# Performance work log

Measured on AMD Instinct MI355X. Metric: run time of the kernel, lower is better.

Reference implementation:

```python
import jax, jax.numpy as jnp
import numpy as np


def setup_inputs() -> dict:
    B, L, D, M, S = 4, 1024, 1024, 16, 8
    key = jax.random.key(0)
    ks = jax.random.split(key, 12)
    sd = 0.02
    inp = {
        "hid": jax.random.normal(ks[0], (B, L, D), jnp.float32),
        "src_hid": jax.random.normal(ks[1], (B, L, D), jnp.float32),
        "sp_width": jax.random.randint(ks[2], (B, L), 0, 9),
        "max_sp_len": S,
        "attention_mask": jnp.ones((B, L), bool),
        "src_mask": jnp.ones((B, L), bool),
        # span-start attention (1 head): query/key linears + relative-key embedding table
        "wq_st": sd * jax.random.normal(ks[3], (D, D), jnp.float32),
        "bq_st": jnp.zeros((D,), jnp.float32),
        "wk_st": sd * jax.random.normal(ks[4], (D, D), jnp.float32),
        "bk_st": jnp.zeros((D,), jnp.float32),
        "rel_st": sd * jax.random.normal(ks[5], (2 * M + 1, D), jnp.float32),
        # span-end attention
        "wq_ed": sd * jax.random.normal(ks[6], (D, D), jnp.float32),
        "bq_ed": jnp.zeros((D,), jnp.float32),
        "wk_ed": sd * jax.random.normal(ks[7], (D, D), jnp.float32),
        "bk_ed": jnp.zeros((D,), jnp.float32),
        "rel_ed": sd * jax.random.normal(ks[8], (2 * M + 1, D), jnp.float32),
        # sp_emb: Linear(2D -> D), stored as [2D, D] (x @ W + b)
        "sp_w": sd * jax.random.normal(ks[9], (2 * D, D), jnp.float32),
        "sp_b": jnp.zeros((D,), jnp.float32),
    }
    return inp


def reference(hid, src_hid, sp_width, max_sp_len, attention_mask, src_mask,
              wq_st, bq_st, wk_st, bk_st, rel_st,
              wq_ed, bq_ed, wk_ed, bk_ed, rel_ed, sp_w, sp_b):
    B, L, D = hid.shape
    scale = 1.0 / jnp.sqrt(jnp.float32(D))
    M = (rel_st.shape[0] - 1) // 2
    pos = jnp.arange(L)
    rel_idx = jnp.clip(pos[None, :] - pos[:, None], -M, M) + M          # [L,L]
    rel_idx_b = jnp.broadcast_to(rel_idx[None], (B, L, L))

    amask = (src_mask[:, :, None] & attention_mask[:, None, :]).astype(jnp.float32)  # [B,Lq,Lk]
    attn_w0 = amask / jnp.clip(jnp.sum(amask, 2, keepdims=True), 1e-6)

    def attn(query, wq, bq, wk, bk, rel_tab, mask):
        # single-head relative-position attention; returns attention weights [B,L,L]
        q = (query @ wq + bq) * scale                                   # [B,L,D]
        k = hid @ wk + bk                                               # [B,L,D]
        sc = jnp.einsum('bqd,bkd->bqk', q, k)
        # q . rel_emb[rel_idx[q_pos,k_pos]]: contract with table then gather (avoids [L,L,D])
        rel_sc = jnp.take_along_axis(jnp.einsum('bqd,rd->bqr', q, rel_tab), rel_idx_b, axis=2)
        sc = jnp.where(mask > 0, sc + rel_sc, -1e18)
        return jax.nn.softmax(sc, axis=-1)

    def upd(attn_w, hidp):
        # weighted sum of hid + linear + relu (dropout is identity in eval)
        hidc = jnp.einsum('bqk,bkd->bqd', attn_w, hid)
        return jax.nn.relu(jnp.concatenate([hidp, hidc], axis=2) @ sp_w + sp_b)

    sts, eds, masks = [attn_w0], [attn_w0], []
    hid1, hid2 = src_hid, src_hid
    for i in range(max_sp_len):
        m = (i < sp_width).astype(jnp.float32)                          # [B,L]
        masks.append(m)
        mask_i = m[:, :, None] * amask                                  # [B,L,L]
        hid1 = upd(sts[-1], hid1)
        sts.append(attn(hid1, wq_st, bq_st, wk_st, bk_st, rel_st, mask_i))
        hid2 = upd(eds[-1], hid2)
        eds.append(attn(hid2, wq_ed, bq_ed, wk_ed, bk_ed, rel_ed, mask_i))

    return (jnp.stack(sts[1:], -2),   # [B,L,S,L]
            jnp.stack(eds[1:], -2),   # [B,L,S,L]
            jnp.stack(masks, -1))     # [B,L,S]
```

## Files before the change

kernel.cpp:

```cpp
#include <hip/hip_runtime.h>

typedef unsigned short u16;
typedef __attribute__((ext_vector_type(8))) short bh8;
typedef __attribute__((ext_vector_type(4))) float f4;

__device__ __forceinline__ u16 f2b(float x){
  union { float f; unsigned u; } c; c.f = x;
  unsigned r = (c.u + 0x7FFFu + ((c.u >> 16) & 1u)) >> 16;
  return (u16)r;
}
__device__ __forceinline__ float b2f(u16 h){
  union { unsigned u; float f; } c; c.u = ((unsigned)h) << 16; return c.f;
}
__device__ __forceinline__ void gload16(const void* g, void* l){
  __builtin_amdgcn_global_load_lds((const __attribute__((address_space(1))) void*)g,
                                   (__attribute__((address_space(3))) void*)l, 16, 0, 0);
}


__global__ __launch_bounds__(256) void convall_k(const float* __restrict__ hid,
                                                 const float* __restrict__ wq0, const float* __restrict__ wq1,
                                                 const float* __restrict__ wk0, const float* __restrict__ wk1,
                                                 u16* __restrict__ hidB, u16* __restrict__ wqB, u16* __restrict__ wkB){
  long i = (long)blockIdx.x*256 + threadIdx.x;
  const float* src; u16* dst; long off;
  if      (i < 4194304L){ src = hid; dst = hidB;           off = i; }
  else if (i < 5242880L){ src = wq0; dst = wqB;            off = i - 4194304L; }
  else if (i < 6291456L){ src = wq1; dst = wqB + 1048576;  off = i - 5242880L; }
  else if (i < 7340032L){ src = wk0; dst = wkB;            off = i - 6291456L; }
  else                  { src = wk1; dst = wkB + 1048576;  off = i - 7340032L; }
  dst[off] = f2b(src[off]);
}

__global__ __launch_bounds__(256) void uniform0_k(const int* __restrict__ spw, float* __restrict__ out){
  int bl = blockIdx.x;
  if (spw[bl] != 0) return;
  f4 t = {0.0009765625f, 0.0009765625f, 0.0009765625f, 0.0009765625f};
  float* b0 = out + (size_t)bl*8192;
  float* b1 = out + 33554432ull + (size_t)bl*8192;
  #pragma unroll
  for (int i = 0; i < 8; i++){
    ((f4*)(b0 + (size_t)i*1024))[threadIdx.x] = t;
    ((f4*)(b1 + (size_t)i*1024))[threadIdx.x] = t;
  }
}

__global__ __launch_bounds__(256) void trans_k(const float* __restrict__ in, u16* __restrict__ out,
                                               int R, int C){
  __shared__ u16 t[32][33];
  int bx = blockIdx.x*32, by = blockIdx.y*32;
  int tx = threadIdx.x & 31, ty = threadIdx.x >> 5;
  #pragma unroll
  for (int j = 0; j < 32; j += 8) t[ty+j][tx] = f2b(in[(size_t)(by+ty+j)*C + bx+tx]);
  __syncthreads();
  #pragma unroll
  for (int j = 0; j < 32; j += 8) out[(size_t)(bx+ty+j)*R + by+tx] = t[tx][ty+j];
}

__global__ __launch_bounds__(256) void sort_k(const int* __restrict__ spw, int* __restrict__ perm,
                                              int* __restrict__ cnt, float* __restrict__ mout){
  int b = blockIdx.x, t = threadIdx.x;
  __shared__ int hist[9], start[9];
  if (t < 9) hist[t] = 0;
  __syncthreads();
  for (int l = t; l < 1024; l += 256) atomicAdd(&hist[spw[b*1024 + l]], 1);
  __syncthreads();
  if (t == 0){
    int acc = 0;
    for (int w = 8; w >= 0; w--){ start[w] = acc; acc += hist[w]; }
  }
  __syncthreads();
  if (t < 8) cnt[b*8 + t] = start[t];
  __syncthreads();
  for (int l = t; l < 1024; l += 256){
    int w = spw[b*1024 + l];
    float* mo = mout + ((size_t)b*1024 + l)*8;
    #pragma unroll
    for (int i = 0; i < 8; i++) mo[i] = (i < w) ? 1.0f : 0.0f;
    int pos = atomicAdd(&start[w], 1);
    perm[b*1024 + pos] = l;
  }
}

__global__ __launch_bounds__(256) void gather_k(const float* __restrict__ srch, const int* __restrict__ perm,
                                                u16* __restrict__ hb){
  int blk = blockIdx.x;
  int z = blk >> 10, c = blk & 1023;
  int ro = perm[z*1024 + c];
  const float* src = srch + ((size_t)z*1024 + ro)*1024;
  u16* dst = hb + ((size_t)z*1024 + c)*1024;
  for (int d = threadIdx.x; d < 1024; d += 256) dst[d] = f2b(src[d]);
}

__global__ __launch_bounds__(256) void wrt_k(const float* __restrict__ wq0, const float* __restrict__ wq1,
                                             const float* __restrict__ rel0, const float* __restrict__ rel1,
                                             u16* __restrict__ Mx){
  long idx = (long)blockIdx.x*256 + threadIdx.x;
  if (idx >= 2L*33*1024) return;
  int s = idx >= 33*1024; long loc = idx - (s ? 33*1024 : 0);
  int r = (int)(loc >> 10), e = (int)(loc & 1023);
  const float* wqrow = (s ? wq1 : wq0) + (size_t)e*1024;
  const float* rel = (s ? rel1 : rel0) + (size_t)r*1024;
  float acc = 0.0f;
  #pragma unroll 4
  for (int k = 0; k < 1024; k++) acc += wqrow[k]*rel[k];
  u16 v = f2b(acc*0.03125f);
  size_t o = (size_t)(1024 + r)*1024 + e;
  #pragma unroll
  for (int b = 0; b < 4; b++)
    Mx[(size_t)(s*4 + b)*1179648 + o] = v;
}

__global__ __launch_bounds__(256) void dots_k(const float* __restrict__ wq0, const float* __restrict__ wq1,
                                              const float* __restrict__ wk0, const float* __restrict__ wk1,
                                              const float* __restrict__ bq0, const float* __restrict__ bq1,
                                              const float* __restrict__ bk0, const float* __restrict__ bk1,
                                              const float* __restrict__ rel0, const float* __restrict__ rel1,
                                              float* __restrict__ ubuf, float* __restrict__ c0buf,
                                              float* __restrict__ bqbk, float* __restrict__ cba){
  int row = blockIdx.x*4 + (threadIdx.x >> 6);
  int lane = threadIdx.x & 63;
  if (row >= 4164) return;
  const float *a, *v;
  int kind = 0, oi = 0, br_s = 0, br_r = 0;
  if      (row < 1024){ a = wk0 + (size_t)row*1024; v = bq0; oi = row; }
  else if (row < 2048){ a = wk1 + (size_t)(row-1024)*1024; v = bq1; oi = row; }
  else if (row < 3072){ a = wq0 + (size_t)(row-2048)*1024; v = bk0; kind = 1; oi = row-2048; }
  else if (row < 4096){ a = wq1 + (size_t)(row-3072)*1024; v = bk1; kind = 1; oi = row-3072+1024; }
  else if (row < 4162){ int idx = row-4096; br_s = idx/33; br_r = idx%33;
                        a = (br_s ? rel1 : rel0) + (size_t)br_r*1024; v = br_s ? bq1 : bq0; kind = 2; }
  else                { int s2 = row-4162; a = s2 ? bq1 : bq0; v = s2 ? bk1 : bk0; kind = 3; oi = s2; }
  const f4* ap = (const f4*)a;
  const f4* vp = (const f4*)v;
  float acc = 0.0f;
  #pragma unroll
  for (int p = 0; p < 4; p++){
    f4 x = ap[lane + 64*p], y = vp[lane + 64*p];
    acc += x[0]*y[0] + x[1]*y[1] + x[2]*y[2] + x[3]*y[3];
  }
  #pragma unroll
  for (int off = 32; off > 0; off >>= 1) acc += __shfl_xor(acc, off, 64);
  if (lane == 0){
    if (kind == 0) ubuf[oi] = acc;
    else if (kind == 1) c0buf[oi] = acc;
    else if (kind == 2){
      float w = acc*0.03125f;
      for (int b = 0; b < 4; b++) cba[(br_s*4 + b)*1152 + 1024 + br_r] = w;
    } else bqbk[oi] = acc;
  }
}

__global__ __launch_bounds__(256) void cba_k(const float* __restrict__ hid, const float* __restrict__ u,
                                             const float* __restrict__ bqbk, float* __restrict__ cba){
  int row = blockIdx.x*4 + (threadIdx.x >> 6);
  int lane = threadIdx.x & 63;
  int z = row >> 10, l = row & 1023, b = z & 3, s = z >> 2;
  const f4* hp = (const f4*)(hid + ((size_t)b*1024 + l)*1024);
  const f4* up = (const f4*)(u + s*1024);
  float acc = 0.0f;
  #pragma unroll
  for (int p = 0; p < 4; p++){
    f4 a = hp[lane + 64*p], c = up[lane + 64*p];
    acc += a[0]*c[0] + a[1]*c[1] + a[2]*c[2] + a[3]*c[3];
  }
  #pragma unroll
  for (int off = 32; off > 0; off >>= 1) acc += __shfl_xor(acc, off, 64);
  if (!lane) cba[z*1152 + l] = (acc + bqbk[s])*0.03125f;
}

__global__ __launch_bounds__(256) void meanh2_k(const u16* __restrict__ H2T, float* __restrict__ mh){
  int row = blockIdx.x*4 + (threadIdx.x >> 6);
  int lane = threadIdx.x & 63;
  const u16* p = H2T + (size_t)row*1024 + lane*16;
  float s = 0.0f;
  #pragma unroll
  for (int j = 0; j < 16; j++) s += b2f(p[j]);
  #pragma unroll
  for (int off = 32; off > 0; off >>= 1) s += __shfl_xor(s, off, 64);
  if (lane == 0) mh[row] = s * 0.0009765625f;
}

__global__ __launch_bounds__(256) void softmax_k(const u16* __restrict__ scB, float* __restrict__ outF,
                                                 u16* __restrict__ attnP, const float* __restrict__ qrelb,
                                                 const int* __restrict__ cnt, const int* __restrict__ perm,
                                                 const int* __restrict__ spw, int iter){
  int z = blockIdx.x >> 10, c = blockIdx.x & 1023;
  int s = z >> 2, b = z & 3;
  if (c >= cnt[b*8 + iter]) return;
  int ro = perm[b*1024 + c];
  __shared__ float qr[33];
  __shared__ float red[8];
  if (threadIdx.x < 33) qr[threadIdx.x] = qrelb[((size_t)z*1024 + c)*33 + threadIdx.x];
  __syncthreads();
  const u16* sc = scB + ((size_t)z*1024 + c)*1024;
  float* po = outF + (size_t)s*33554432ull + (((size_t)(b*1024 + ro))*8 + (size_t)iter)*1024;
  u16* pr = attnP + ((size_t)z*1024 + c)*1024;
  int t = threadIdx.x;
  float v[4]; float mx = -1e30f;
  #pragma unroll
  for (int j = 0; j < 4; j++){
    int col = t + j*256;
    int d = col - ro; d = d < -16 ? -16 : (d > 16 ? 16 : d);
    v[j] = b2f(sc[col]) + qr[d + 16];
    mx = fmaxf(mx, v[j]);
  }
  #pragma unroll
  for (int off = 32; off > 0; off >>= 1) mx = fmaxf(mx, __shfl_xor(mx, off, 64));
  int wv = t >> 6, ln = t & 63;
  if (ln == 0) red[wv] = mx;
  __syncthreads();
  mx = fmaxf(fmaxf(red[0], red[1]), fmaxf(red[2], red[3]));
  float sm = 0.0f;
  #pragma unroll
  for (int j = 0; j < 4; j++){ v[j] = __expf(v[j] - mx); sm += v[j]; }
  #pragma unroll
  for (int off = 32; off > 0; off >>= 1) sm += __shfl_xor(sm, off, 64);
  if (ln == 0) red[4 + wv] = sm;
  __syncthreads();
  sm = red[4] + red[5] + red[6] + red[7];
  float inv = 1.0f / sm;
  #pragma unroll
  for (int j = 0; j < 4; j++){
    float pv = v[j] * inv;
    po[t + j*256] = pv;
    pr[t + j*256] = f2b(pv);
  }
  int w = spw[b*1024 + ro];
  if (iter == w - 1 && w < 8){
    f4 u = {0.0009765625f, 0.0009765625f, 0.0009765625f, 0.0009765625f};
    for (int j = 1; j <= 7 - iter; j++)
      ((f4*)(po + (size_t)j*1024))[t] = u;
  }
}

template<int MODE>
__global__ __launch_bounds__(256) void gemm_k(
    const u16* __restrict__ A_, const u16* __restrict__ B_,
    const u16* __restrict__ A2_, const u16* __restrict__ B2_,
    const float* __restrict__ e0, const float* __restrict__ e1,
    u16* __restrict__ outB, u16* __restrict__ outB2, float* __restrict__ qrelb,
    const int* __restrict__ cnt, int iter, int azmask)
{
  const int z = blockIdx.z;
  const size_t LD = 1024*1024;
  const int bm = blockIdx.y*128, bn = blockIdx.x*128;
  int s = z >> 2, b = z & 3;
  bool m5h2 = false;
  if constexpr (MODE == 5){ if (z >= 8){ m5h2 = true; b = z - 8; s = 0; } }

  int cntv = 1024;
  if constexpr (MODE == 2 || MODE == 4){
    cntv = cnt[b*8 + iter];
    if (bm >= cntv) return;
  }

  const u16 *A1, *B1, *A2, *B2;
  int lda1 = 1024, ldb1 = 1024, lda2 = 1024, ldb2 = 1024, K = 1024, K1 = 1024;

  if constexpr (MODE == 0){ A1 = A_ + (size_t)z*LD; B1 = B_ + (size_t)z*LD; A2=A1; B2=B1; }
  else if constexpr (MODE == 2){
    A1 = A_ + (size_t)z*LD; B1 = B_ + (size_t)b*LD;
    A2 = A2_ + (size_t)(z & azmask)*LD; B2 = B2_; ldb2 = 2048;
    if (iter == 0){ K = 1024; K1 = 0; } else { K = 2048; K1 = 1024; }
  }
  else if constexpr (MODE == 4){ A1 = A_ + (size_t)(z & azmask)*LD; B1 = B_ + (size_t)z*1179648; A2=A1; B2=B1; }
  else {
    if (!m5h2){ A1 = A_ + (size_t)b*LD; B1 = B_ + (size_t)s*LD; }
    else      { A1 = A2_ + 1024; lda1 = 2048; B1 = B2_ + (size_t)b*LD; }
    A2=A1; B2=B1; lda2=lda1;
  }

  __shared__ __align__(16) u16 lA[16384];
  __shared__ __align__(16) u16 lB[16384];
  const int tid = threadIdx.x, wv = tid >> 6, lane = tid & 63;
  const int wr = (wv >> 1)*64, wc = (wv & 1)*64;
  const int fr = lane & 15, kh = lane >> 4;
  const int stRow = (lane >> 2);
  const int ssw  = ((lane >> 2) & 3) ^ ((lane >> 4) & 3);
  const int stCe = ((lane & 3) ^ ssw)*8;
  const int fsw  = (fr & 3) ^ ((fr >> 2) & 3);
  const int rdSl = (kh ^ fsw)*8;

  auto stage = [&](int bufsel, int k0s){
    const u16 *As, *Bs; int kk, la, lb;
    if (k0s < K1){ As = A1; Bs = B1; kk = k0s; la = lda1; lb = ldb1; }
    else         { As = A2; Bs = B2; kk = k0s - K1; la = lda2; lb = ldb2; }
    #pragma unroll
    for (int c = 0; c < 4; c++){
      const int n = wv*4 + c;
      const int h = n >> 3;
      const int rl = (n & 7)*16 + stRow;
      const int ke = kk + h*32 + stCe;
      gload16(As + (size_t)(bm + rl)*la + ke, (char*)lA + bufsel*16384 + n*1024);
      gload16(Bs + (size_t)(bn + rl)*lb + ke, (char*)lB + bufsel*16384 + n*1024);
    }
  };

  f4 acc[4][4];
  #pragma unroll
  for (int i = 0; i < 4; i++)
    #pragma unroll
    for (int j = 0; j < 4; j++)
      acc[i][j] = f4{0.f, 0.f, 0.f, 0.f};

  stage(0, 0);
  stage(1, 64);

  int cur = 0;
  for (int k0 = 0; k0 < K; k0 += 64){
    if (k0 + 64 < K) asm volatile("s_waitcnt vmcnt(8)" ::: "memory");
    else             asm volatile("s_waitcnt vmcnt(0)" ::: "memory");
    __builtin_amdgcn_s_barrier();
    asm volatile("" ::: "memory");
    const u16* bufA = lA + cur*8192;
    const u16* bufB = lB + cur*8192;
    bh8 af[2][4], bfr[2][4];
    #pragma unroll
    for (int h = 0; h < 2; h++){
      #pragma unroll
      for (int i = 0; i < 4; i++){
        af[h][i]  = *(const bh8*)&bufA[h*4096 + (wr + i*16 + fr)*32 + rdSl];
        bfr[h][i] = *(const bh8*)&bufB[h*4096 + (wc + i*16 + fr)*32 + rdSl];
      }
    }
    if (k0 + 128 < K){
      asm volatile("s_waitcnt lgkmcnt(0)" ::: "memory");
      __builtin_amdgcn_sched_barrier(0);
      __builtin_amdgcn_s_barrier();
      asm volatile("" ::: "memory");
      stage(cur, k0 + 128);
    }
    __builtin_amdgcn_s_setprio(1);
    #pragma unroll
    for (int h = 0; h < 2; h++)
      #pragma unroll
      for (int i = 0; i < 4; i++)
        #pragma unroll
        for (int j = 0; j < 4; j++)
          acc[i][j] = __builtin_amdgcn_mfma_f32_16x16x32_bf16(af[h][i], bfr[h][j], acc[i][j], 0, 0, 0);
    __builtin_amdgcn_s_setprio(0);
    cur ^= 1;
  }

  const int rw = (lane >> 4)*4, cl = lane & 15;
  #pragma unroll
  for (int i = 0; i < 4; i++){
    #pragma unroll
    for (int r = 0; r < 4; r++){
      const int row = bm + wr + i*16 + rw + r;
      if constexpr (MODE == 2 || MODE == 4){ if (row >= cntv) continue; }
      #pragma unroll
      for (int j = 0; j < 4; j++){
        const int col = bn + wc + j*16 + cl;
        float v = acc[i][j][r];
        if constexpr (MODE == 0){
          outB[(size_t)z*LD + (size_t)row*1024 + col] = f2b(v);
        } else if constexpr (MODE == 2){
          v += e0[col];
          if (e1) v += e1[b*1024 + col];
          v = fmaxf(v, 0.0f);
          outB[(size_t)z*LD + (size_t)row*1024 + col] = f2b(v);
        } else if constexpr (MODE == 5){
          if (!m5h2)
            outB[(size_t)z*1179648 + (size_t)row*1024 + col] = f2b((v + e0[s*1024 + col])*0.03125f);
          else
            outB2[(size_t)b*LD + (size_t)row*1024 + col] = f2b(v);
        } else {
          v += e0[z*1152 + col];
          if (col < 1024){
            outB[((size_t)z*1024 + row)*1024 + col] = f2b(v);
          } else {
            int rr = col - 1024;
            if (rr < 33) qrelb[((size_t)z*1024 + row)*33 + rr] = v;
          }
        }
      }
    }
  }
}


extern "C" void kernel_launch(void* const* d_in, const int* in_sizes, int n_in,
                              void* d_out, int out_size, void* d_ws, size_t ws_size,
                              hipStream_t stream)
{
  const float* hid    = (const float*)d_in[0];
  const float* srch   = (const float*)d_in[1];
  const int*   spw    = (const int*)d_in[2];
  const float* wq_st  = (const float*)d_in[6];
  const float* bq_st  = (const float*)d_in[7];
  const float* wk_st  = (const float*)d_in[8];
  const float* bk_st  = (const float*)d_in[9];
  const float* rel_st = (const float*)d_in[10];
  const float* wq_ed  = (const float*)d_in[11];
  const float* bq_ed  = (const float*)d_in[12];
  const float* wk_ed  = (const float*)d_in[13];
  const float* bk_ed  = (const float*)d_in[14];
  const float* rel_ed = (const float*)d_in[15];
  const float* sp_w   = (const float*)d_in[16];
  const float* sp_b   = (const float*)d_in[17];
  float* out = (float*)d_out;

  const size_t LD = 1024*1024;
  char* p = (char*)d_ws;
  u16* hidB  = (u16*)p; p += 4*LD*2;
  u16* wqB   = (u16*)p; p += 2*LD*2;
  u16* wkB   = (u16*)p; p += 2*LD*2;
  u16* spwT  = (u16*)p; p += 2*LD*2;
  u16* WT    = (u16*)p; p += 2*LD*2;
  u16* H2T   = (u16*)p; p += 4*LD*2;
  u16* Mx    = (u16*)p; p += 8ull*1179648*2;
  u16* attnP = (u16*)p; p += 8*LD*2;
  u16* hbufA = (u16*)p; p += 8*LD*2;
  u16* hbufB = (u16*)p; p += 8*LD*2;
  u16* scB   = (u16*)p; p += 8*LD*2;
  float* qrelb  = (float*)p; p += 8*1024*33*4;
  float* cba    = (float*)p; p += 8*1152*4;
  float* ubuf   = (float*)p; p += 2048*4;
  float* c0buf  = (float*)p; p += 2048*4;
  float* bqbk   = (float*)p; p += 64;
  float* meanH2 = (float*)p; p += 4*1024*4;
  int*   perm   = (int*)p;   p += 4*1024*4;
  int*   cnt    = (int*)p;   p += 1024;

  const dim3 t256(256);

  convall_k<<<32768, t256, 0, stream>>>(hid, wq_st, wq_ed, wk_st, wk_ed, hidB, wqB, wkB);
  sort_k<<<4, t256, 0, stream>>>(spw, perm, cnt, out + 67108864ull);
  gather_k<<<4096, t256, 0, stream>>>(srch, perm, hbufA);
  uniform0_k<<<4096, t256, 0, stream>>>(spw, out);
  trans_k<<<dim3(32,64), t256, 0, stream>>>(sp_w, spwT, 2048, 1024);
  wrt_k<<<264, t256, 0, stream>>>(wq_st, wq_ed, rel_st, rel_ed, Mx);
  dots_k<<<1041, t256, 0, stream>>>(wq_st, wq_ed, wk_st, wk_ed, bq_st, bq_ed, bk_st, bk_ed,
                                    rel_st, rel_ed, ubuf, c0buf, bqbk, cba);
  cba_k<<<2048, t256, 0, stream>>>(hid, ubuf, bqbk, cba);

  gemm_k<0><<<dim3(8,8,2), t256, 0, stream>>>(wqB, wkB, nullptr, nullptr, nullptr, nullptr,
                                              WT, nullptr, nullptr, nullptr, 0, 7);
  gemm_k<5><<<dim3(8,8,12), t256, 0, stream>>>(hidB, WT, spwT, hidB, c0buf, nullptr,
                                               Mx, H2T, nullptr, nullptr, 0, 7);
  meanh2_k<<<1024, t256, 0, stream>>>(H2T, meanH2);

  u16* hp = hbufA; u16* hn = hbufB;
  for (int i = 0; i < 8; i++){
    int g2z = (i == 0) ? 4 : 8;
    int am2 = (i <= 1) ? 3 : 7;
    gemm_k<2><<<dim3(8,8,g2z), t256, 0, stream>>>(attnP, H2T, hp, spwT, sp_b,
                                                  (i == 0) ? meanH2 : nullptr,
                                                  hn, nullptr, nullptr, cnt, i, am2);
    int am4 = (i == 0) ? 3 : 7;
    gemm_k<4><<<dim3(9,8,8), t256, 0, stream>>>(hn, Mx, nullptr, nullptr, cba, nullptr,
                                                scB, nullptr, qrelb, cnt, i, am4);
    softmax_k<<<8192, t256, 0, stream>>>(scB, out, attnP, qrelb, cnt, perm, spw, i);
    u16* tmp = hp; hp = hn; hn = tmp;
  }
}
```

Measured before the change: 909.0 us.

## Fold rel-table projection into MFMA gemm and vectorize bf16 conversion

Removes the scalar wrt_k kernel, which computed the Wq·rel products with naive per-thread fp32 dot products. That work now runs as extra z-slices of the MODE 0 MFMA GEMM, reading a bf16 copy of the rel tables. The conversion kernel is vectorized to four floats per thread and also converts the rel tables. The trade-off is that the rel projection is now computed in bf16 instead of fp32, and the extra GEMM slices use 128-row tiles of which only 33 rows are valid.

```diff
diff --git a/kernel.cpp b/kernel.cpp
--- a/kernel.cpp
+++ b/kernel.cpp
@@ -21,15 +21,22 @@
 __global__ __launch_bounds__(256) void convall_k(const float* __restrict__ hid,
                                                  const float* __restrict__ wq0, const float* __restrict__ wq1,
                                                  const float* __restrict__ wk0, const float* __restrict__ wk1,
-                                                 u16* __restrict__ hidB, u16* __restrict__ wqB, u16* __restrict__ wkB){
-  long i = (long)blockIdx.x*256 + threadIdx.x;
+                                                 const float* __restrict__ rel0, const float* __restrict__ rel1,
+                                                 u16* __restrict__ hidB, u16* __restrict__ wqB,
+                                                 u16* __restrict__ wkB, u16* __restrict__ relB){
+  long g = (long)blockIdx.x*256 + threadIdx.x;
+  if (g >= 2114048L) return;
   const float* src; u16* dst; long off;
-  if      (i < 4194304L){ src = hid; dst = hidB;           off = i; }
-  else if (i < 5242880L){ src = wq0; dst = wqB;            off = i - 4194304L; }
-  else if (i < 6291456L){ src = wq1; dst = wqB + 1048576;  off = i - 5242880L; }
-  else if (i < 7340032L){ src = wk0; dst = wkB;            off = i - 6291456L; }
-  else                  { src = wk1; dst = wkB + 1048576;  off = i - 7340032L; }
-  dst[off] = f2b(src[off]);
+  if      (g < 1048576L){ src = hid;  dst = hidB;           off = g; }
+  else if (g < 1310720L){ src = wq0;  dst = wqB;            off = g - 1048576L; }
+  else if (g < 1572864L){ src = wq1;  dst = wqB + 1048576;  off = g - 1310720L; }
+  else if (g < 1835008L){ src = wk0;  dst = wkB;            off = g - 1572864L; }
+  else if (g < 2097152L){ src = wk1;  dst = wkB + 1048576;  off = g - 1835008L; }
+  else if (g < 2105600L){ src = rel0; dst = relB;           off = g - 2097152L; }
+  else                  { src = rel1; dst = relB + 131072;  off = g - 2105600L; }
+  f4 v = *(const f4*)(src + off*4);
+  ushort4 pk = make_ushort4(f2b(v[0]), f2b(v[1]), f2b(v[2]), f2b(v[3]));
+  *(ushort4*)(dst + off*4) = pk;
 }
 
 __global__ __launch_bounds__(256) void uniform0_k(const int* __restrict__ spw, float* __restrict__ out){
@@ -90,25 +97,6 @@
   const float* src = srch + ((size_t)z*1024 + ro)*1024;
   u16* dst = hb + ((size_t)z*1024 + c)*1024;
   for (int d = threadIdx.x; d < 1024; d += 256) dst[d] = f2b(src[d]);
-}
-
-__global__ __launch_bounds__(256) void wrt_k(const float* __restrict__ wq0, const float* __restrict__ wq1,
-                                             const float* __restrict__ rel0, const float* __restrict__ rel1,
-                                             u16* __restrict__ Mx){
-  long idx = (long)blockIdx.x*256 + threadIdx.x;
-  if (idx >= 2L*33*1024) return;
-  int s = idx >= 33*1024; long loc = idx - (s ? 33*1024 : 0);
-  int r = (int)(loc >> 10), e = (int)(loc & 1023);
-  const float* wqrow = (s ? wq1 : wq0) + (size_t)e*1024;
-  const float* rel = (s ? rel1 : rel0) + (size_t)r*1024;
-  float acc = 0.0f;
-  #pragma unroll 4
-  for (int k = 0; k < 1024; k++) acc += wqrow[k]*rel[k];
-  u16 v = f2b(acc*0.03125f);
-  size_t o = (size_t)(1024 + r)*1024 + e;
-  #pragma unroll
-  for (int b = 0; b < 4; b++)
-    Mx[(size_t)(s*4 + b)*1179648 + o] = v;
 }
 
 __global__ __launch_bounds__(256) void dots_k(const float* __restrict__ wq0, const float* __restrict__ wq1,
@@ -257,7 +245,15 @@
   const u16 *A1, *B1, *A2, *B2;
   int lda1 = 1024, ldb1 = 1024, lda2 = 1024, ldb2 = 1024, K = 1024, K1 = 1024;
 
-  if constexpr (MODE == 0){ A1 = A_ + (size_t)z*LD; B1 = B_ + (size_t)z*LD; A2=A1; B2=B1; }
+  if constexpr (MODE == 0){
+    if (z < 2){ A1 = A_ + (size_t)z*LD; B1 = B_ + (size_t)z*LD; }
+    else {
+      if (blockIdx.y > 0) return;
+      A1 = A2_ + (size_t)(z-2)*131072;
+      B1 = A_ + (size_t)(z-2)*LD;
+    }
+    A2=A1; B2=B1;
+  }
   else if constexpr (MODE == 2){
     A1 = A_ + (size_t)z*LD; B1 = B_ + (size_t)b*LD;
     A2 = A2_ + (size_t)(z & azmask)*LD; B2 = B2_; ldb2 = 2048;
@@ -354,7 +350,16 @@
         const int col = bn + wc + j*16 + cl;
         float v = acc[i][j][r];
         if constexpr (MODE == 0){
-          outB[(size_t)z*LD + (size_t)row*1024 + col] = f2b(v);
+          if (z < 2){
+            outB[(size_t)z*LD + (size_t)row*1024 + col] = f2b(v);
+          } else if (row < 33){
+            u16 vv = f2b(v*0.03125f);
+            size_t o = (size_t)(1024 + row)*1024 + col;
+            int sx = z - 2;
+            #pragma unroll
+            for (int bb = 0; bb < 4; bb++)
+              outB2[(size_t)(sx*4 + bb)*1179648 + o] = vv;
+          }
         } else if constexpr (MODE == 2){
           v += e0[col];
           if (e1) v += e1[b*1024 + col];
@@ -406,6 +411,7 @@
   u16* hidB  = (u16*)p; p += 4*LD*2;
   u16* wqB   = (u16*)p; p += 2*LD*2;
   u16* wkB   = (u16*)p; p += 2*LD*2;
+  u16* relB  = (u16*)p; p += 2*131072*2;
   u16* spwT  = (u16*)p; p += 2*LD*2;
   u16* WT    = (u16*)p; p += 2*LD*2;
   u16* H2T   = (u16*)p; p += 4*LD*2;
@@ -425,18 +431,18 @@
 
   const dim3 t256(256);
 
-  convall_k<<<32768, t256, 0, stream>>>(hid, wq_st, wq_ed, wk_st, wk_ed, hidB, wqB, wkB);
+  convall_k<<<8258, t256, 0, stream>>>(hid, wq_st, wq_ed, wk_st, wk_ed, rel_st, rel_ed,
+                                       hidB, wqB, wkB, relB);
   sort_k<<<4, t256, 0, stream>>>(spw, perm, cnt, out + 67108864ull);
   gather_k<<<4096, t256, 0, stream>>>(srch, perm, hbufA);
   uniform0_k<<<4096, t256, 0, stream>>>(spw, out);
   trans_k<<<dim3(32,64), t256, 0, stream>>>(sp_w, spwT, 2048, 1024);
-  wrt_k<<<264, t256, 0, stream>>>(wq_st, wq_ed, rel_st, rel_ed, Mx);
   dots_k<<<1041, t256, 0, stream>>>(wq_st, wq_ed, wk_st, wk_ed, bq_st, bq_ed, bk_st, bk_ed,
                                     rel_st, rel_ed, ubuf, c0buf, bqbk, cba);
   cba_k<<<2048, t256, 0, stream>>>(hid, ubuf, bqbk, cba);
 
-  gemm_k<0><<<dim3(8,8,2), t256, 0, stream>>>(wqB, wkB, nullptr, nullptr, nullptr, nullptr,
-                                              WT, nullptr, nullptr, nullptr, 0, 7);
+  gemm_k<0><<<dim3(8,8,4), t256, 0, stream>>>(wqB, wkB, relB, nullptr, nullptr, nullptr,
+                                              WT, Mx, nullptr, nullptr, 0, 7);
   gemm_k<5><<<dim3(8,8,12), t256, 0, stream>>>(hidB, WT, spwT, hidB, c0buf, nullptr,
                                                Mx, H2T, nullptr, nullptr, 0, 7);
   meanh2_k<<<1024, t256, 0, stream>>>(H2T, meanH2);
```

New measurement: 820.7 us (median of 2 runs). -9.7%, faster.
